# Kernel optimization log

Hardware: AMD Instinct MI355X
Metric: run time of the kernel (lower is better)

The kernel has to match this reference:

```python
import jax, jax.numpy as jnp
import numpy as np

D_MODEL = 1024
NUM_HEADS = 16
DEPTH = D_MODEL // NUM_HEADS


def setup_inputs() -> dict:
    key = jax.random.key(0)
    ks = jax.random.split(key, 5)
    s = 1.0 / np.sqrt(D_MODEL)
    return {
        "x": jax.random.normal(ks[0], (4, 2048, D_MODEL), dtype=jnp.float32),
        "wq": jax.random.normal(ks[1], (D_MODEL, D_MODEL), dtype=jnp.float32) * s,
        "bq": jnp.zeros((D_MODEL,), dtype=jnp.float32),
        "wk": jax.random.normal(ks[2], (D_MODEL, D_MODEL), dtype=jnp.float32) * s,
        "bk": jnp.zeros((D_MODEL,), dtype=jnp.float32),
        "wv": jax.random.normal(ks[3], (D_MODEL, D_MODEL), dtype=jnp.float32) * s,
        "bv": jnp.zeros((D_MODEL,), dtype=jnp.float32),
        "wo": jax.random.normal(ks[4], (D_MODEL, D_MODEL), dtype=jnp.float32) * s,
        "bo": jnp.zeros((D_MODEL,), dtype=jnp.float32),
    }


def reference(x, wq, bq, wk, bk, wv, bv, wo, bo):
    B, S, _ = x.shape
    def split_heads(t):  # [B,S,D] -> [B,H,S,depth]
        return t.reshape(B, S, NUM_HEADS, DEPTH).transpose(0, 2, 1, 3)
    q = split_heads(x @ wq + bq)
    k = split_heads(x @ wk + bk)
    v = split_heads(x @ wv + bv)
    scale = 1.0 / jnp.sqrt(jnp.float32(DEPTH))
    logits = jnp.einsum("bhqd,bhkd->bhqk", q, k) * scale
    attn = jax.nn.softmax(logits, axis=-1)  # dropout is identity at inference
    out = jnp.einsum("bhqk,bhkd->bhqd", attn, v)
    out = out.transpose(0, 2, 1, 3).reshape(B, S, D_MODEL)
    return out @ wo + bo
```

## Files before the change

### kernel.cpp

```cpp
#include <hip/hip_runtime.h>
#include <hip/hip_bf16.h>
#include <cstdint>
#include <cstddef>

typedef __attribute__((ext_vector_type(8))) short s8v;
typedef __attribute__((ext_vector_type(4))) float f4v;
typedef __attribute__((ext_vector_type(16))) float f16v;
typedef __attribute__((ext_vector_type(4))) unsigned u4v;

#define MFMA_BF16(a, b, c) __builtin_amdgcn_mfma_f32_16x16x32_bf16((a), (b), (c), 0, 0, 0)
#define MFMA32(a, b, c) __builtin_amdgcn_mfma_f32_32x32x16_bf16((a), (b), (c), 0, 0, 0)

__device__ __forceinline__ short f2bf(float f) {
    unsigned u = __builtin_bit_cast(unsigned, f);
    u += 0x7FFFu + ((u >> 16) & 1u);
    return (short)(u >> 16);
}

__device__ __forceinline__ unsigned cvt_pk_bf16(float a, float b) {
    unsigned r;
    asm("v_cvt_pk_bf16_f32 %0, %1, %2" : "=v"(r) : "v"(a), "v"(b));
    return r;
}

#define GLDS16(gsrc, ldst)                                                                   \
    __builtin_amdgcn_global_load_lds(                                                        \
        (const __attribute__((address_space(1))) unsigned int*)(gsrc),                       \
        (__attribute__((address_space(3))) unsigned int*)(ldst), 16, 0, 0)

__global__ void convert_x(const float4* __restrict__ in, short4* __restrict__ out, int n4) {
    int i = blockIdx.x * blockDim.x + threadIdx.x;
    int stride = gridDim.x * blockDim.x;
    for (; i < n4; i += stride) {
        float4 v = in[i];
        short4 o;
        o.x = f2bf(v.x); o.y = f2bf(v.y); o.z = f2bf(v.z); o.w = f2bf(v.w);
        out[i] = o;
    }
}

__global__ void transpose_w(const float* __restrict__ a0, const float* __restrict__ a1,
                            const float* __restrict__ a2, const float* __restrict__ a3,
                            short* __restrict__ outb) {
    const float* src = (blockIdx.z == 0) ? a0 : (blockIdx.z == 1) ? a1 : (blockIdx.z == 2) ? a2 : a3;
    short* dst = outb + (size_t)blockIdx.z * 1048576;
    __shared__ float t[32][33];
    const int n0 = blockIdx.x * 32, k0 = blockIdx.y * 32;
    const int tid = threadIdx.x;
    const int rr = tid >> 3, c4 = (tid & 7) * 4;
    float4 v = *(const float4*)(src + (size_t)(k0 + rr) * 1024 + n0 + c4);
    t[rr][c4 + 0] = v.x; t[rr][c4 + 1] = v.y; t[rr][c4 + 2] = v.z; t[rr][c4 + 3] = v.w;
    __syncthreads();
    short4 o;
    o.x = f2bf(t[c4 + 0][rr]); o.y = f2bf(t[c4 + 1][rr]);
    o.z = f2bf(t[c4 + 2][rr]); o.w = f2bf(t[c4 + 3][rr]);
    *(short4*)(dst + (size_t)(n0 + rr) * 1024 + k0 + c4) = o;
}

__global__ __launch_bounds__(256, 2) void qkv_gemm(const short* __restrict__ xb,
                                                   const short* __restrict__ wT,
                                                   const float* __restrict__ bq,
                                                   const float* __restrict__ bk,
                                                   const float* __restrict__ bv,
                                                   short* __restrict__ qb,
                                                   short* __restrict__ kblk,
                                                   short* __restrict__ vtb,
                                                   float qscale) {
    __shared__ short As[128 * 64];
    __shared__ short Bs[128 * 64];
    const int z = blockIdx.x % 3;
    const int bxx = blockIdx.x / 3;
    const int tid = threadIdx.x;
    const int lane = tid & 63;
    const int w = tid >> 6;
    const int wr = w >> 1, wc = w & 1;
    int m0, n0;
    const short *A, *B;
    if (z < 2) { A = xb; B = wT + z * 1048576; m0 = blockIdx.y * 128; n0 = bxx * 128; }
    else       { A = wT + 2 * 1048576; B = xb; m0 = bxx * 128; n0 = blockIdx.y * 128; }

    f4v acc[4][4] = {};

    for (int kt = 0; kt < 1024; kt += 64) {
#pragma unroll
        for (int i = 0; i < 4; i++) {
            int o = tid * 16 + i * 4096;
            int r = o >> 7;
            int cs = (o & 127) ^ ((r & 7) << 4);
            GLDS16((const char*)A + (size_t)(m0 + r) * 2048 + kt * 2 + cs,
                   (char*)As + (w * 1024 + i * 4096));
            GLDS16((const char*)B + (size_t)(n0 + r) * 2048 + kt * 2 + cs,
                   (char*)Bs + (w * 1024 + i * 4096));
        }
        __syncthreads();
#pragma unroll
        for (int kk = 0; kk < 2; kk++) {
            s8v af[4], bf[4];
#pragma unroll
            for (int mi = 0; mi < 4; mi++) {
                int r = wr * 64 + mi * 16 + (lane & 15);
                int cb = (((lane >> 4) * 16) + kk * 64) ^ ((r & 7) << 4);
                af[mi] = *(const s8v*)((const char*)As + r * 128 + cb);
            }
#pragma unroll
            for (int ni = 0; ni < 4; ni++) {
                int r = wc * 64 + ni * 16 + (lane & 15);
                int cb = (((lane >> 4) * 16) + kk * 64) ^ ((r & 7) << 4);
                bf[ni] = *(const s8v*)((const char*)Bs + r * 128 + cb);
            }
#pragma unroll
            for (int mi = 0; mi < 4; mi++)
#pragma unroll
                for (int ni = 0; ni < 4; ni++)
                    acc[mi][ni] = MFMA_BF16(af[mi], bf[ni], acc[mi][ni]);
        }
        __syncthreads();
    }

#pragma unroll
    for (int mi = 0; mi < 4; mi++) {
#pragma unroll
        for (int ni = 0; ni < 4; ni++) {
            int row = m0 + wr * 64 + mi * 16 + ((lane >> 4) << 2);
            int col = n0 + wc * 64 + ni * 16 + (lane & 15);
#pragma unroll
            for (int j = 0; j < 4; j++) {
                float v = acc[mi][ni][j];
                if (z == 0) {
                    v = (v + bq[col]) * qscale;
                    qb[(size_t)(row + j) * 1024 + col] = f2bf(v);
                } else if (z == 1) {
                    v = v + bk[col];
                    int rs = row + j;
                    int b = rs >> 11, s_in = rs & 2047;
                    int t = s_in >> 6, ktb = (s_in >> 5) & 1, l5v = s_in & 31;
                    int h = col >> 6, dd = col & 63;
                    int st = dd >> 4, Hh = (dd >> 3) & 1, jj = dd & 7;
                    size_t kidx = (size_t)(((b * 16 + h) * 32 + t)) * 4096 +
                                  (ktb * 4 + st) * 512 + (Hh * 32 + l5v) * 8 + jj;
                    kblk[kidx] = f2bf(v);
                } else {
                    v = v + bv[row + j];
                    size_t idx = (size_t)(col >> 11) * (2048 * 1024) + (size_t)(row + j) * 2048 + (col & 2047);
                    vtb[idx] = f2bf(v);
                }
            }
        }
    }
}

__global__ __launch_bounds__(256, 2) void gemm_o(const short* __restrict__ A,
                                                 const short* __restrict__ B,
                                                 const float* __restrict__ bias,
                                                 float* __restrict__ C) {
    __shared__ short As[128 * 64];
    __shared__ short Bs[128 * 64];
    const int tid = threadIdx.x;
    const int lane = tid & 63;
    const int w = tid >> 6;
    const int wr = w >> 1, wc = w & 1;
    const int m0 = blockIdx.y * 128, n0 = blockIdx.x * 128;

    f4v acc[4][4] = {};

    for (int kt = 0; kt < 1024; kt += 64) {
#pragma unroll
        for (int i = 0; i < 4; i++) {
            int o = tid * 16 + i * 4096;
            int r = o >> 7;
            int cs = (o & 127) ^ ((r & 7) << 4);
            GLDS16((const char*)A + (size_t)(m0 + r) * 2048 + kt * 2 + cs,
                   (char*)As + (w * 1024 + i * 4096));
            GLDS16((const char*)B + (size_t)(n0 + r) * 2048 + kt * 2 + cs,
                   (char*)Bs + (w * 1024 + i * 4096));
        }
        __syncthreads();
#pragma unroll
        for (int kk = 0; kk < 2; kk++) {
            s8v af[4], bf[4];
#pragma unroll
            for (int mi = 0; mi < 4; mi++) {
                int r = wr * 64 + mi * 16 + (lane & 15);
                int cb = (((lane >> 4) * 16) + kk * 64) ^ ((r & 7) << 4);
                af[mi] = *(const s8v*)((const char*)As + r * 128 + cb);
            }
#pragma unroll
            for (int ni = 0; ni < 4; ni++) {
                int r = wc * 64 + ni * 16 + (lane & 15);
                int cb = (((lane >> 4) * 16) + kk * 64) ^ ((r & 7) << 4);
                bf[ni] = *(const s8v*)((const char*)Bs + r * 128 + cb);
            }
#pragma unroll
            for (int mi = 0; mi < 4; mi++)
#pragma unroll
                for (int ni = 0; ni < 4; ni++)
                    acc[mi][ni] = MFMA_BF16(af[mi], bf[ni], acc[mi][ni]);
        }
        __syncthreads();
    }

#pragma unroll
    for (int mi = 0; mi < 4; mi++) {
#pragma unroll
        for (int ni = 0; ni < 4; ni++) {
            int row = m0 + wr * 64 + mi * 16 + ((lane >> 4) << 2);
            int col = n0 + wc * 64 + ni * 16 + (lane & 15);
#pragma unroll
            for (int j = 0; j < 4; j++)
                C[(size_t)(row + j) * 1024 + col] = acc[mi][ni][j] + bias[col];
        }
    }
}

__global__ __launch_bounds__(256, 4) void attn_fwd(const short* __restrict__ Qb,
                                                   const short* __restrict__ Kblk,
                                                   const short* __restrict__ Vtb,
                                                   short* __restrict__ AOb) {
    __shared__ short Vs[2][64 * 64];

    const int tid = threadIdx.x, lane = tid & 63, w = tid >> 6;
    const int l5 = lane & 31, H = lane >> 5;
    const int qt = blockIdx.x;
    const int bh = blockIdx.y;
    const int b = bh >> 4, h = bh & 15;
    const int q0 = qt * 128 + w * 32;

    s8v qf[4];
#pragma unroll
    for (int st = 0; st < 4; st++)
        qf[st] = *(const s8v*)(Qb + (size_t)(b * 2048 + q0 + l5) * 1024 + h * 64 + st * 16 + H * 8);

    const short* kbase = Kblk + (size_t)(b * 16 + h) * 131072 + lane * 8;

    f16v oacc[2] = {};
    float l_ = 0.f;

    auto STAGE_V = [&](int s0, int bi) {
#pragma unroll
        for (int i = 0; i < 2; i++) {
            int o = tid * 16 + i * 4096;
            int r = o >> 7;
            int cs = (o & 127) ^ ((r & 7) << 4);
            GLDS16((const char*)Vtb + (size_t)(b * 1024 + h * 64 + r) * 4096 + (size_t)s0 * 2 + cs,
                   (char*)Vs[bi] + w * 1024 + i * 4096);
        }
    };

    STAGE_V(0, 0);
    __syncthreads();

    int cur = 0;
    for (int t = 0; t < 32; t++) {
        if (t < 31) STAGE_V((t + 1) * 64, cur ^ 1);

        s8v kf[2][4];
#pragma unroll
        for (int kt = 0; kt < 2; kt++)
#pragma unroll
            for (int st = 0; st < 4; st++)
                kf[kt][st] = *(const s8v*)(kbase + t * 4096 + (kt * 4 + st) * 512);

        f16v sf[2] = {};
        __builtin_amdgcn_s_setprio(1);
#pragma unroll
        for (int kt = 0; kt < 2; kt++)
#pragma unroll
            for (int st = 0; st < 4; st++)
                sf[kt] = MFMA32(kf[kt][st], qf[st], sf[kt]);
        __builtin_amdgcn_s_setprio(0);

        float rs0 = 0.f, rs1 = 0.f;
#pragma unroll
        for (int kt = 0; kt < 2; kt++)
#pragma unroll
            for (int i = 0; i < 16; i++) {
                float p = __builtin_amdgcn_exp2f(sf[kt][i]);
                sf[kt][i] = p;
                if (i & 1) rs1 += p; else rs0 += p;
            }
        l_ += rs0 + rs1;

#pragma unroll
        for (int s = 0; s < 4; s++) {
            const int kt = s >> 1, base = (s & 1) * 8;
            unsigned dA0 = cvt_pk_bf16(sf[kt][base + 0], sf[kt][base + 1]);
            unsigned dA1 = cvt_pk_bf16(sf[kt][base + 2], sf[kt][base + 3]);
            unsigned dB0 = cvt_pk_bf16(sf[kt][base + 4], sf[kt][base + 5]);
            unsigned dB1 = cvt_pk_bf16(sf[kt][base + 6], sf[kt][base + 7]);
            asm("v_permlane32_swap_b32 %0, %1" : "+v"(dA0), "+v"(dB0));
            asm("v_permlane32_swap_b32 %0, %1" : "+v"(dA1), "+v"(dB1));
            u4v fw = {dA0, dA1, dB0, dB1};
            s8v pfrag = __builtin_bit_cast(s8v, fw);
            __builtin_amdgcn_s_setprio(1);
#pragma unroll
            for (int dt = 0; dt < 2; dt++) {
                int r = dt * 32 + l5;
                s8v vf = *(const s8v*)((const char*)Vs[cur] + r * 128 + ((s * 32 + H * 16) ^ ((r & 7) << 4)));
                oacc[dt] = MFMA32(vf, pfrag, oacc[dt]);
            }
            __builtin_amdgcn_s_setprio(0);
        }
        __syncthreads();
        cur ^= 1;
    }

    float l = l_ + __shfl_xor(l_, 32, 64);
    float rl = 1.0f / l;
    size_t orow = (size_t)(b * 2048 + q0 + l5) * 1024 + h * 64;
#pragma unroll
    for (int dt = 0; dt < 2; dt++)
#pragma unroll
        for (int g = 0; g < 4; g++) {
            short4 o;
            o.x = f2bf(oacc[dt][4 * g + 0] * rl);
            o.y = f2bf(oacc[dt][4 * g + 1] * rl);
            o.z = f2bf(oacc[dt][4 * g + 2] * rl);
            o.w = f2bf(oacc[dt][4 * g + 3] * rl);
            *(short4*)(AOb + orow + dt * 32 + g * 8 + H * 4) = o;
        }
}

extern "C" void kernel_launch(void* const* d_in, const int* in_sizes, int n_in,
                              void* d_out, int out_size, void* d_ws, size_t ws_size,
                              hipStream_t stream) {
    const float* x  = (const float*)d_in[0];
    const float* wq = (const float*)d_in[1];
    const float* bq = (const float*)d_in[2];
    const float* wk = (const float*)d_in[3];
    const float* bk = (const float*)d_in[4];
    const float* wv = (const float*)d_in[5];
    const float* bv = (const float*)d_in[6];
    const float* wo = (const float*)d_in[7];
    const float* bo = (const float*)d_in[8];
    float* out = (float*)d_out;

    char* ws = (char*)d_ws;
    const size_t MB16 = 16777216;
    short* xb   = (short*)(ws);
    short* qb   = (short*)(ws + 1 * MB16);
    short* kblk = (short*)(ws + 2 * MB16);
    short* vtb  = (short*)(ws + 3 * MB16);
    short* wT   = (short*)(ws + 4 * MB16);
    short* aob  = xb;

    const float qscale = 0.125f * 1.4426950408889634f;

    convert_x<<<dim3(1024), dim3(256), 0, stream>>>((const float4*)x, (short4*)xb, 8388608 / 4);
    transpose_w<<<dim3(32, 32, 4), dim3(256), 0, stream>>>(wq, wk, wv, wo, wT);

    qkv_gemm<<<dim3(24, 64), dim3(256), 0, stream>>>(xb, wT, bq, bk, bv, qb, kblk, vtb, qscale);

    attn_fwd<<<dim3(16, 64), dim3(256), 0, stream>>>(qb, kblk, vtb, aob);

    gemm_o<<<dim3(8, 64), dim3(256), 0, stream>>>(aob, wT + 3 * 1048576, bo, out);
}
```

Before: 198.0 us.

## Store V in MFMA fragment-blocked layout and load directly from global

The QKV GEMM epilogue now writes V into a per-head, per-64-key-tile blocked layout that matches the 32x32 MFMA operand fragments, mirroring the existing K layout. The attention kernel drops the double-buffered LDS staging of V and its per-tile barrier, loading V fragments straight from global memory into registers and reusing the K register array. This removes LDS traffic and synchronisation but relies on L2/cache hits for V reads shared by the four waves and the other query tiles, and exposes global load latency without explicit prefetch.

```diff
diff --git a/kernel.cpp b/kernel.cpp
--- a/kernel.cpp
+++ b/kernel.cpp
@@ -64,7 +64,7 @@
                                                    const float* __restrict__ bv,
                                                    short* __restrict__ qb,
                                                    short* __restrict__ kblk,
-                                                   short* __restrict__ vtb,
+                                                   short* __restrict__ vblk,
                                                    float qscale) {
     __shared__ short As[128 * 64];
     __shared__ short Bs[128 * 64];
@@ -140,9 +140,16 @@
                                   (ktb * 4 + st) * 512 + (Hh * 32 + l5v) * 8 + jj;
                     kblk[kidx] = f2bf(v);
                 } else {
-                    v = v + bv[row + j];
-                    size_t idx = (size_t)(col >> 11) * (2048 * 1024) + (size_t)(row + j) * 2048 + (col & 2047);
-                    vtb[idx] = f2bf(v);
+                    int dfull = row + j;
+                    v = v + bv[dfull];
+                    int h2 = dfull >> 6, dd = dfull & 63;
+                    int dt = dd >> 5, l5v = dd & 31;
+                    int bb = col >> 11, s_in = col & 2047;
+                    int t = s_in >> 6, rem = s_in & 63;
+                    int sfr = rem >> 4, Hh = (rem >> 3) & 1, jj = rem & 7;
+                    size_t vidx = (size_t)(((bb * 16 + h2) * 32 + t)) * 4096 +
+                                  (sfr * 2 + dt) * 512 + (Hh * 32 + l5v) * 8 + jj;
+                    vblk[vidx] = f2bf(v);
                 }
             }
         }
@@ -214,10 +221,8 @@
 
 __global__ __launch_bounds__(256, 4) void attn_fwd(const short* __restrict__ Qb,
                                                    const short* __restrict__ Kblk,
-                                                   const short* __restrict__ Vtb,
+                                                   const short* __restrict__ Vblk,
                                                    short* __restrict__ AOb) {
-    __shared__ short Vs[2][64 * 64];
-
     const int tid = threadIdx.x, lane = tid & 63, w = tid >> 6;
     const int l5 = lane & 31, H = lane >> 5;
     const int qt = blockIdx.x;
@@ -231,34 +236,16 @@
         qf[st] = *(const s8v*)(Qb + (size_t)(b * 2048 + q0 + l5) * 1024 + h * 64 + st * 16 + H * 8);
 
     const short* kbase = Kblk + (size_t)(b * 16 + h) * 131072 + lane * 8;
+    const short* vbase = Vblk + (size_t)(b * 16 + h) * 131072 + lane * 8;
 
     f16v oacc[2] = {};
     float l_ = 0.f;
 
-    auto STAGE_V = [&](int s0, int bi) {
-#pragma unroll
-        for (int i = 0; i < 2; i++) {
-            int o = tid * 16 + i * 4096;
-            int r = o >> 7;
-            int cs = (o & 127) ^ ((r & 7) << 4);
-            GLDS16((const char*)Vtb + (size_t)(b * 1024 + h * 64 + r) * 4096 + (size_t)s0 * 2 + cs,
-                   (char*)Vs[bi] + w * 1024 + i * 4096);
-        }
-    };
-
-    STAGE_V(0, 0);
-    __syncthreads();
-
-    int cur = 0;
     for (int t = 0; t < 32; t++) {
-        if (t < 31) STAGE_V((t + 1) * 64, cur ^ 1);
-
-        s8v kf[2][4];
-#pragma unroll
-        for (int kt = 0; kt < 2; kt++)
-#pragma unroll
-            for (int st = 0; st < 4; st++)
-                kf[kt][st] = *(const s8v*)(kbase + t * 4096 + (kt * 4 + st) * 512);
+        s8v kv[8];
+#pragma unroll
+        for (int f = 0; f < 8; f++)
+            kv[f] = *(const s8v*)(kbase + t * 4096 + f * 512);
 
         f16v sf[2] = {};
         __builtin_amdgcn_s_setprio(1);
@@ -266,8 +253,12 @@
         for (int kt = 0; kt < 2; kt++)
 #pragma unroll
             for (int st = 0; st < 4; st++)
-                sf[kt] = MFMA32(kf[kt][st], qf[st], sf[kt]);
+                sf[kt] = MFMA32(kv[kt * 4 + st], qf[st], sf[kt]);
         __builtin_amdgcn_s_setprio(0);
+
+#pragma unroll
+        for (int f = 0; f < 8; f++)
+            kv[f] = *(const s8v*)(vbase + t * 4096 + f * 512);
 
         float rs0 = 0.f, rs1 = 0.f;
 #pragma unroll
@@ -293,15 +284,10 @@
             s8v pfrag = __builtin_bit_cast(s8v, fw);
             __builtin_amdgcn_s_setprio(1);
 #pragma unroll
-            for (int dt = 0; dt < 2; dt++) {
-                int r = dt * 32 + l5;
-                s8v vf = *(const s8v*)((const char*)Vs[cur] + r * 128 + ((s * 32 + H * 16) ^ ((r & 7) << 4)));
-                oacc[dt] = MFMA32(vf, pfrag, oacc[dt]);
-            }
+            for (int dt = 0; dt < 2; dt++)
+                oacc[dt] = MFMA32(kv[s * 2 + dt], pfrag, oacc[dt]);
             __builtin_amdgcn_s_setprio(0);
         }
-        __syncthreads();
-        cur ^= 1;
     }
 
     float l = l_ + __shfl_xor(l_, 32, 64);
@@ -339,7 +325,7 @@
     short* xb   = (short*)(ws);
     short* qb   = (short*)(ws + 1 * MB16);
     short* kblk = (short*)(ws + 2 * MB16);
-    short* vtb  = (short*)(ws + 3 * MB16);
+    short* vblk = (short*)(ws + 3 * MB16);
     short* wT   = (short*)(ws + 4 * MB16);
     short* aob  = xb;
 
@@ -348,9 +334,9 @@
     convert_x<<<dim3(1024), dim3(256), 0, stream>>>((const float4*)x, (short4*)xb, 8388608 / 4);
     transpose_w<<<dim3(32, 32, 4), dim3(256), 0, stream>>>(wq, wk, wv, wo, wT);
 
-    qkv_gemm<<<dim3(24, 64), dim3(256), 0, stream>>>(xb, wT, bq, bk, bv, qb, kblk, vtb, qscale);
-
-    attn_fwd<<<dim3(16, 64), dim3(256), 0, stream>>>(qb, kblk, vtb, aob);
+    qkv_gemm<<<dim3(24, 64), dim3(256), 0, stream>>>(xb, wT, bq, bk, bv, qb, kblk, vblk, qscale);
+
+    attn_fwd<<<dim3(16, 64), dim3(256), 0, stream>>>(qb, kblk, vblk, aob);
 
     gemm_o<<<dim3(8, 64), dim3(256), 0, stream>>>(aob, wT + 3 * 1048576, bo, out);
 }
```

Measured after the change: 201.0 us. No clear change (+1.5%).

## Stage K tiles through swizzled LDS instead of per-wave global blocked loads

Applied to the files above, without the earlier changes.

K is now written row-major by the QKV GEMM instead of in a pre-blocked MFMA-fragment layout. The attention kernel stages each 64-row K tile into double-buffered, XOR-swizzled shared memory alongside V, and reads MFMA operands from LDS. This shares each K tile across the four waves rather than having every wave fetch it from global memory, and it simplifies the K store scatter. In exchange it doubles LDS use per block, which may limit occupancy, and adds LDS read traffic.

```diff
diff --git a/kernel.cpp b/kernel.cpp
--- a/kernel.cpp
+++ b/kernel.cpp
@@ -63,7 +63,7 @@
                                                    const float* __restrict__ bk,
                                                    const float* __restrict__ bv,
                                                    short* __restrict__ qb,
-                                                   short* __restrict__ kblk,
+                                                   short* __restrict__ kb,
                                                    short* __restrict__ vtb,
                                                    float qscale) {
     __shared__ short As[128 * 64];
@@ -131,14 +131,7 @@
                     qb[(size_t)(row + j) * 1024 + col] = f2bf(v);
                 } else if (z == 1) {
                     v = v + bk[col];
-                    int rs = row + j;
-                    int b = rs >> 11, s_in = rs & 2047;
-                    int t = s_in >> 6, ktb = (s_in >> 5) & 1, l5v = s_in & 31;
-                    int h = col >> 6, dd = col & 63;
-                    int st = dd >> 4, Hh = (dd >> 3) & 1, jj = dd & 7;
-                    size_t kidx = (size_t)(((b * 16 + h) * 32 + t)) * 4096 +
-                                  (ktb * 4 + st) * 512 + (Hh * 32 + l5v) * 8 + jj;
-                    kblk[kidx] = f2bf(v);
+                    kb[(size_t)(row + j) * 1024 + col] = f2bf(v);
                 } else {
                     v = v + bv[row + j];
                     size_t idx = (size_t)(col >> 11) * (2048 * 1024) + (size_t)(row + j) * 2048 + (col & 2047);
@@ -213,9 +206,10 @@
 }
 
 __global__ __launch_bounds__(256, 4) void attn_fwd(const short* __restrict__ Qb,
-                                                   const short* __restrict__ Kblk,
+                                                   const short* __restrict__ Kb,
                                                    const short* __restrict__ Vtb,
                                                    short* __restrict__ AOb) {
+    __shared__ short Ks[2][64 * 64];
     __shared__ short Vs[2][64 * 64];
 
     const int tid = threadIdx.x, lane = tid & 63, w = tid >> 6;
@@ -230,43 +224,41 @@
     for (int st = 0; st < 4; st++)
         qf[st] = *(const s8v*)(Qb + (size_t)(b * 2048 + q0 + l5) * 1024 + h * 64 + st * 16 + H * 8);
 
-    const short* kbase = Kblk + (size_t)(b * 16 + h) * 131072 + lane * 8;
-
     f16v oacc[2] = {};
     float l_ = 0.f;
 
-    auto STAGE_V = [&](int s0, int bi) {
+    auto STAGE = [&](int s0, int bi) {
 #pragma unroll
         for (int i = 0; i < 2; i++) {
             int o = tid * 16 + i * 4096;
             int r = o >> 7;
             int cs = (o & 127) ^ ((r & 7) << 4);
+            GLDS16((const char*)Kb + (size_t)(b * 2048 + s0 + r) * 2048 + h * 128 + cs,
+                   (char*)Ks[bi] + w * 1024 + i * 4096);
             GLDS16((const char*)Vtb + (size_t)(b * 1024 + h * 64 + r) * 4096 + (size_t)s0 * 2 + cs,
                    (char*)Vs[bi] + w * 1024 + i * 4096);
         }
     };
 
-    STAGE_V(0, 0);
+    STAGE(0, 0);
     __syncthreads();
 
     int cur = 0;
     for (int t = 0; t < 32; t++) {
-        if (t < 31) STAGE_V((t + 1) * 64, cur ^ 1);
-
-        s8v kf[2][4];
-#pragma unroll
-        for (int kt = 0; kt < 2; kt++)
-#pragma unroll
-            for (int st = 0; st < 4; st++)
-                kf[kt][st] = *(const s8v*)(kbase + t * 4096 + (kt * 4 + st) * 512);
+        if (t < 31) STAGE((t + 1) * 64, cur ^ 1);
 
         f16v sf[2] = {};
         __builtin_amdgcn_s_setprio(1);
 #pragma unroll
-        for (int kt = 0; kt < 2; kt++)
-#pragma unroll
-            for (int st = 0; st < 4; st++)
-                sf[kt] = MFMA32(kf[kt][st], qf[st], sf[kt]);
+        for (int kt = 0; kt < 2; kt++) {
+            int r = kt * 32 + l5;
+            int swz = (r & 7) << 4;
+#pragma unroll
+            for (int st = 0; st < 4; st++) {
+                s8v kf = *(const s8v*)((const char*)Ks[cur] + r * 128 + ((st * 32 + H * 16) ^ swz));
+                sf[kt] = MFMA32(kf, qf[st], sf[kt]);
+            }
+        }
         __builtin_amdgcn_s_setprio(0);
 
         float rs0 = 0.f, rs1 = 0.f;
@@ -336,21 +328,21 @@
 
     char* ws = (char*)d_ws;
     const size_t MB16 = 16777216;
-    short* xb   = (short*)(ws);
-    short* qb   = (short*)(ws + 1 * MB16);
-    short* kblk = (short*)(ws + 2 * MB16);
-    short* vtb  = (short*)(ws + 3 * MB16);
-    short* wT   = (short*)(ws + 4 * MB16);
-    short* aob  = xb;
+    short* xb  = (short*)(ws);
+    short* qb  = (short*)(ws + 1 * MB16);
+    short* kb  = (short*)(ws + 2 * MB16);
+    short* vtb = (short*)(ws + 3 * MB16);
+    short* wT  = (short*)(ws + 4 * MB16);
+    short* aob = xb;
 
     const float qscale = 0.125f * 1.4426950408889634f;
 
     convert_x<<<dim3(1024), dim3(256), 0, stream>>>((const float4*)x, (short4*)xb, 8388608 / 4);
     transpose_w<<<dim3(32, 32, 4), dim3(256), 0, stream>>>(wq, wk, wv, wo, wT);
 
-    qkv_gemm<<<dim3(24, 64), dim3(256), 0, stream>>>(xb, wT, bq, bk, bv, qb, kblk, vtb, qscale);
-
-    attn_fwd<<<dim3(16, 64), dim3(256), 0, stream>>>(qb, kblk, vtb, aob);
+    qkv_gemm<<<dim3(24, 64), dim3(256), 0, stream>>>(xb, wT, bq, bk, bv, qb, kb, vtb, qscale);
+
+    attn_fwd<<<dim3(16, 64), dim3(256), 0, stream>>>(qb, kb, vtb, aob);
 
     gemm_o<<<dim3(8, 64), dim3(256), 0, stream>>>(aob, wT + 3 * 1048576, bo, out);
 }
```

Result: no change. 195.9 us (-1.1%).
